# Kernel tuning notes

Hardware: AMD Instinct MI355X
Metric: run time of the kernel (lower is better)

## Reference

```python
import jax, jax.numpy as jnp
import numpy as np

B, S, H, F, E, K = 4, 2048, 1024, 3584, 8, 2
CAP_FACTOR = 1.25


def setup_inputs() -> dict:
    key = jax.random.key(0)
    k1, k2, k3, k4, k5 = jax.random.split(key, 5)
    s_h = 1.0 / np.sqrt(H)
    s_f = 1.0 / np.sqrt(F)
    return {
        "hidden_states": jax.random.normal(k1, (B, S, H), dtype=jnp.float32),
        "gate_w": jax.random.normal(k2, (E, H), dtype=jnp.float32) * s_h,
        "w1": jax.random.normal(k3, (E, H, F), dtype=jnp.float32) * s_h,
        "w2": jax.random.normal(k4, (E, F, H), dtype=jnp.float32) * s_f,
        "w3": jax.random.normal(k5, (E, H, F), dtype=jnp.float32) * s_h,
    }


def _moe_forward(hidden_states, gate_w, w1, w2, w3):
    b, s, h = hidden_states.shape
    dtype = hidden_states.dtype
    x = hidden_states.reshape(-1, h)  # [B*S, H]
    router_logits = x @ gate_w.T  # [B*S, E]
    expert_weights = jax.nn.softmax(router_logits.astype(jnp.float32), axis=1)
    _, selected_experts = jax.lax.top_k(expert_weights, K)  # [B*S, K]

    top_k_idx = selected_experts.reshape(b, s, K)
    probs = expert_weights.reshape(b, s, E)

    capacity = int(s * K / E * CAP_FACTOR)  # expert capacity per batch

    # dispatch/combine masks (Mixtral 'dropping' implementation)
    expert_mask = jax.nn.one_hot(top_k_idx, E, dtype=jnp.int32)  # [b,s,K,E]
    mask_fused = expert_mask.reshape(b, s * K, E)
    count_fused = jnp.cumsum(mask_fused, axis=1)  # running count per expert
    count = count_fused.reshape(b, s, K, E)
    trunc_mask = expert_mask * (count <= capacity).astype(jnp.int32)
    combined_mask = trunc_mask.sum(axis=2)  # [b,s,E]
    masked_probs = probs * combined_mask  # drop over-capacity tokens

    pos_fused = mask_fused * count_fused
    pos = pos_fused.reshape(b, s, K, E)
    combined_pos = pos.sum(axis=2) * combined_mask  # [b,s,E], 1-based slot
    pos_in_cap = jax.nn.one_hot(combined_pos, capacity + 1, dtype=jnp.int32)
    combine_mask = masked_probs[..., None] * pos_in_cap  # [b,s,E,cap+1]
    combine_mask = combine_mask[..., 1:].astype(dtype)  # drop slot 0 (dropped tokens)
    dispatch_mask = (combine_mask != 0).astype(dtype)  # [b,s,E,cap]

    # dispatch tokens into per-expert capacity buffers
    dispatch = jnp.einsum('bsm,bsec->ebcm', hidden_states, dispatch_mask)
    # expert FFN (SwiGLU)
    h1 = jnp.einsum('ebcm,emh->ebch', dispatch, w1)
    h3 = jnp.einsum('ebcm,emh->ebch', dispatch, w3)
    expert_out = jnp.einsum('ebch,ehm->ebcm', jax.nn.silu(h1) * h3, w2)
    # combine back to token order with routing probabilities
    final = jnp.einsum('ebcm,bsec->bsm', expert_out, combine_mask)
    return final


def reference(hidden_states, gate_w, w1, w2, w3):
    return _moe_forward(hidden_states, gate_w, w1, w2, w3)
```

## Files before the change

kernel.cpp:

```cpp
#include <hip/hip_runtime.h>
#include <hip/hip_bf16.h>
#include <math.h>

#define B_   4
#define S_   2048
#define H_   1024
#define F_   3584
#define E_   8
#define TOPK 2
#define CAP  640
#define M_   (B_*CAP)
#define NTOK (B_*S_)

typedef __attribute__((ext_vector_type(8))) short short8;
typedef __attribute__((ext_vector_type(4))) float f32x4;
typedef __attribute__((ext_vector_type(4))) unsigned short us4;

static __device__ __forceinline__ unsigned short f2bf(float f) {
  __hip_bfloat16 h = __float2bfloat16(f);
  return *reinterpret_cast<unsigned short*>(&h);
}
static __device__ __forceinline__ float bf2f(unsigned short u) {
  unsigned int x = ((unsigned int)u) << 16;
  float f;
  __builtin_memcpy(&f, &x, 4);
  return f;
}

static __device__ __forceinline__ void gload16(const void* g, void* l) {
  __builtin_amdgcn_global_load_lds((const __attribute__((address_space(1))) void*)g,
                                   (__attribute__((address_space(3))) void*)l, 16, 0, 0);
}

#define BAR() __builtin_amdgcn_s_barrier()
#define VM4() asm volatile("s_waitcnt vmcnt(4)" ::: "memory")
#define VM0() asm volatile("s_waitcnt vmcnt(0)" ::: "memory")

__global__ __launch_bounds__(64) void k_router(const float* __restrict__ hs,
                                               const float* __restrict__ gw,
                                               int* __restrict__ e01,
                                               float* __restrict__ p01,
                                               unsigned short* __restrict__ hsb) {
  int t = blockIdx.x;
  int lane = threadIdx.x;
  const float4* xv = (const float4*)(hs + (size_t)t * H_);
  float4 xr[4];
#pragma unroll
  for (int i = 0; i < 4; ++i) xr[i] = xv[lane + i * 64];
#pragma unroll
  for (int i = 0; i < 4; ++i) {
    us4 v = {f2bf(xr[i].x), f2bf(xr[i].y), f2bf(xr[i].z), f2bf(xr[i].w)};
    *(us4*)&hsb[(size_t)t * H_ + (size_t)(lane + i * 64) * 4] = v;
  }
  float logit[E_];
#pragma unroll
  for (int e = 0; e < E_; ++e) {
    const float4* gv = (const float4*)(gw + (size_t)e * H_);
    float acc = 0.f;
#pragma unroll
    for (int i = 0; i < 4; ++i) {
      float4 g = gv[lane + i * 64];
      acc += xr[i].x * g.x + xr[i].y * g.y + xr[i].z * g.z + xr[i].w * g.w;
    }
#pragma unroll
    for (int off = 32; off > 0; off >>= 1) acc += __shfl_xor(acc, off);
    logit[e] = acc;
  }
  float mx = logit[0];
#pragma unroll
  for (int e = 1; e < E_; ++e) mx = fmaxf(mx, logit[e]);
  float p[E_], s = 0.f;
#pragma unroll
  for (int e = 0; e < E_; ++e) { p[e] = expf(logit[e] - mx); s += p[e]; }
  float inv = 1.f / s;
  int e0 = 0;
#pragma unroll
  for (int e = 1; e < E_; ++e) if (p[e] > p[e0]) e0 = e;
  int e1 = (e0 == 0) ? 1 : 0;
#pragma unroll
  for (int e = 0; e < E_; ++e) if (e != e0 && p[e] > p[e1]) e1 = e;
  if (lane == 0) {
    e01[t * 2 + 0] = e0;
    e01[t * 2 + 1] = e1;
    p01[t * 2 + 0] = p[e0] * inv;
    p01[t * 2 + 1] = p[e1] * inv;
  }
}

__global__ __launch_bounds__(256) void k_positions(const int* __restrict__ e01,
                                                   int* __restrict__ pos,
                                                   int* __restrict__ disp) {
  int b = blockIdx.x, tid = threadIdx.x;
  __shared__ unsigned char eid[S_ * TOPK];
  __shared__ int part[256];
  for (int i = tid; i < E_ * CAP; i += 256)
    disp[((size_t)(i / CAP) * B_ + b) * CAP + (i % CAP)] = -1;
  for (int i = tid; i < S_ * TOPK; i += 256)
    eid[i] = (unsigned char)e01[b * S_ * TOPK + i];
  __syncthreads();
  const int per = (S_ * TOPK) / 256;
  int base = tid * per;
  for (int e = 0; e < E_; ++e) {
    int cnt = 0;
    for (int j = 0; j < per; ++j) cnt += (eid[base + j] == e) ? 1 : 0;
    part[tid] = cnt;
    __syncthreads();
    for (int off = 1; off < 256; off <<= 1) {
      int v = part[tid];
      int add = (tid >= off) ? part[tid - off] : 0;
      __syncthreads();
      part[tid] = v + add;
      __syncthreads();
    }
    int run = part[tid] - cnt;
    for (int j = 0; j < per; ++j) {
      int sl = base + j;
      if (eid[sl] == e) {
        ++run;
        int p = (run <= CAP) ? (run - 1) : -1;
        pos[b * S_ * TOPK + sl] = p;
        if (p >= 0) disp[((size_t)e * B_ + b) * CAP + p] = sl >> 1;
      }
    }
    __syncthreads();
  }
}

__global__ __launch_bounds__(256) void k_transpose(const float* __restrict__ in,
                                                   unsigned short* __restrict__ outp,
                                                   int R, int C, int ileave, int half,
                                                   size_t ostride_e) {
  __shared__ unsigned short ls[64][72];
  int e = blockIdx.z, tc = blockIdx.x, tr = blockIdx.y, tid = threadIdx.x;
  const float* src = in + (size_t)e * R * C + (size_t)tr * 64 * C + (size_t)tc * 64;
#pragma unroll
  for (int i = 0; i < 16; ++i) {
    int row = i * 4 + (tid >> 6), col = tid & 63;
    ls[row][col] = f2bf(src[(size_t)row * C + col]);
  }
  __syncthreads();
  unsigned short* dbase = outp + (size_t)e * ostride_e;
#pragma unroll
  for (int i = 0; i < 4; ++i) {
    int orow = i * 16 + (tid >> 4), oc = (tid & 15) * 4;
    int gr = tc * 64 + orow;
    int ri = ileave ? ((gr & ~15) * 2 + (gr & 15) + half * 16) : gr;
    us4 v = {ls[oc + 0][orow], ls[oc + 1][orow], ls[oc + 2][orow], ls[oc + 3][orow]};
    *(us4*)&dbase[(size_t)ri * R + tr * 64 + oc] = v;
  }
}

#define STAGE_A(d, h, t) {                                                    \
    size_t _o = (size_t)(t) * 64 + (h) * 32;                                  \
    gload16(pA0 + _o, &lds[((d) * 2 + (h)) * 8192 + tid * 8]);                \
    gload16(pA1 + _o, &lds[((d) * 2 + (h)) * 8192 + tid * 8 + 4096]);         \
  }
#define STAGE_B(d, h, t) {                                                    \
    size_t _o = (size_t)(t) * 64 + (h) * 32;                                  \
    gload16(srcB + _o, &lds[32768 + ((d) * 2 + (h)) * 8192 + tid * 8]);       \
    gload16(srcB + (size_t)128 * KTOT + _o, &lds[32768 + ((d) * 2 + (h)) * 8192 + tid * 8 + 4096]); \
  }
#define RD_A4(d, h, mh) {                                                     \
    const unsigned short* _pa = &lds[((d) * 2 + (h)) * 8192 + aoff + (mh) * 2048]; \
    _Pragma("unroll") for (int j = 0; j < 4; ++j)                             \
      a[j] = *(const short8*)&_pa[j * 512];                                   \
  }
#define RD_B4(d, h) {                                                         \
    const unsigned short* _pb = &lds[32768 + ((d) * 2 + (h)) * 8192 + boff];  \
    _Pragma("unroll") for (int n = 0; n < 4; ++n)                             \
      b[n] = *(const short8*)&_pb[n * 512];                                   \
  }
#define MFMA16(mh) {                                                          \
    __builtin_amdgcn_s_setprio(1);                                            \
    _Pragma("unroll") for (int j = 0; j < 4; ++j)                             \
      _Pragma("unroll") for (int n = 0; n < 4; ++n)                           \
        acc[(mh) * 4 + j][n] = __builtin_amdgcn_mfma_f32_16x16x32_bf16(a[j], b[n], acc[(mh) * 4 + j][n], 0, 0, 0); \
    __builtin_amdgcn_s_setprio(0);                                            \
  }
#define BODY(P, tn) {                                                         \
    RD_A4(P, 0, 0); RD_B4(P, 0); STAGE_A((P) ^ 1, 0, tn); STAGE_B((P) ^ 1, 0, tn); \
    MFMA16(0);                                                                \
    RD_A4(P, 0, 1); MFMA16(1); VM4(); BAR();                                  \
    RD_A4(P, 1, 0); RD_B4(P, 1); STAGE_A((P) ^ 1, 1, tn); STAGE_B((P) ^ 1, 1, tn); \
    MFMA16(0);                                                                \
    RD_A4(P, 1, 1); MFMA16(1); VM4(); BAR();                                  \
  }
#define PEEL(P) {                                                             \
    RD_A4(P, 0, 0); RD_B4(P, 0);                                              \
    MFMA16(0);                                                                \
    RD_A4(P, 0, 1); MFMA16(1); VM0(); BAR();                                  \
    RD_A4(P, 1, 0); RD_B4(P, 1);                                              \
    MFMA16(0);                                                                \
    RD_A4(P, 1, 1); MFMA16(1);                                                \
  }

template <int KTOT, bool SWIGLU, bool GATHER, int MT, int NTN, int NTOTB, int SPLITK>
__global__ __launch_bounds__(512, 2) void k_gemm256(const unsigned short* __restrict__ Aall,
                                                    const unsigned short* __restrict__ Ball,
                                                    unsigned short* __restrict__ Cout,
                                                    const int* __restrict__ disp) {
  constexpr int KSUB = KTOT / SPLITK;
  constexpr int NT = KSUB / 64;
  __shared__ __align__(16) unsigned short lds[65536];

  const int nwg = MT * NTN * E_ * SPLITK;
  int lid = blockIdx.x;
  int sw = (lid & 7) * (nwg >> 3) + (lid >> 3);
  constexpr int PER = MT * NTN;
  int ks = sw / (PER * E_);
  int rem2 = sw - ks * (PER * E_);
  int e = rem2 / PER;
  int rem = rem2 - e * PER;
  int tn = rem / MT, tm = rem - tn * MT;

  int tid = threadIdx.x, li = tid & 63, wid = tid >> 6;
  int wm = wid >> 2, wn = wid & 3;

  int rS = tid >> 2;
  int gS = (tid & 3) ^ ((tid >> 3) & 3);
  const unsigned short* pA0;
  const unsigned short* pA1;
  if constexpr (GATHER) {
    int r0 = tm * 256 + rS;
    int r1 = r0 + 128;
    int b0 = r0 / CAP, b1 = r1 / CAP;
    int tok0 = disp[(size_t)e * B_ * CAP + r0];
    int tok1 = disp[(size_t)e * B_ * CAP + r1];
    if (tok0 < 0) tok0 = 0;
    if (tok1 < 0) tok1 = 0;
    pA0 = Aall + ((size_t)b0 * S_ + tok0) * H_ + ks * KSUB + gS * 8;
    pA1 = Aall + ((size_t)b1 * S_ + tok1) * H_ + ks * KSUB + gS * 8;
  } else {
    const unsigned short* srcA = Aall + ((size_t)e * M_ + (size_t)tm * 256 + rS) * KTOT + ks * KSUB + gS * 8;
    pA0 = srcA;
    pA1 = srcA + (size_t)128 * KTOT;
  }
  const unsigned short* srcB = Ball + ((size_t)e * NTOTB + (size_t)tn * 256 + rS) * KTOT + ks * KSUB + gS * 8;

  int sA = (li >> 4) ^ ((li >> 1) & 3);
  int aoff = (wm * 128 + (li & 15)) * 32 + sA * 8;
  int boff = (wn * 64 + (li & 15)) * 32 + sA * 8;

  f32x4 acc[8][4] = {};
  short8 a[4], b[4];

  STAGE_A(0, 0, 0); STAGE_B(0, 0, 0);
  STAGE_A(0, 1, 0); STAGE_B(0, 1, 0);
  VM4();
  BAR();

#pragma unroll 1
  for (int t = 0; t + 1 < NT - 1; t += 2) {
    BODY(0, t + 1);
    BODY(1, t + 2);
  }
  if constexpr (((NT - 1) & 1) != 0) {
    BODY(0, NT - 1);
  }
  if constexpr (((NT - 1) & 1) != 0) {
    PEEL(1);
  } else {
    PEEL(0);
  }

  int r0o = tm * 256 + wm * 128 + ((li >> 4) << 2);
  if constexpr (SWIGLU) {
    unsigned short* out = Cout + (size_t)e * M_ * F_;
#pragma unroll
    for (int m = 0; m < 8; ++m)
#pragma unroll
      for (int u = 0; u < 2; ++u) {
        int col = (tn * 8 + wn * 2 + u) * 16 + (li & 15);
#pragma unroll
        for (int j = 0; j < 4; ++j) {
          float h1 = acc[m][2 * u][j], h3 = acc[m][2 * u + 1][j];
          float sg = 1.f / (1.f + __expf(-h1));
          out[(size_t)(r0o + m * 16 + j) * F_ + col] = f2bf(h1 * sg * h3);
        }
      }
  } else {
    unsigned short* out = Cout + ((size_t)ks * E_ + e) * M_ * NTOTB;
#pragma unroll
    for (int m = 0; m < 8; ++m)
#pragma unroll
      for (int n = 0; n < 4; ++n) {
        int col = tn * 256 + wn * 64 + n * 16 + (li & 15);
#pragma unroll
        for (int j = 0; j < 4; ++j)
          out[(size_t)(r0o + m * 16 + j) * NTOTB + col] = f2bf(acc[m][n][j]);
      }
  }
}

__global__ __launch_bounds__(256) void k_combine(const unsigned short* __restrict__ Oe0,
                                                 const unsigned short* __restrict__ Oe1,
                                                 const int* __restrict__ e01,
                                                 const float* __restrict__ p01,
                                                 const int* __restrict__ pos,
                                                 float* __restrict__ outp) {
  int t = blockIdx.x;
  int b = t / S_;
  int tid = threadIdx.x;
  float4 acc = {0.f, 0.f, 0.f, 0.f};
#pragma unroll
  for (int k = 0; k < TOPK; ++k) {
    int p = pos[t * 2 + k];
    if (p >= 0) {
      int e = e01[t * 2 + k];
      float w = p01[t * 2 + k];
      size_t row = (size_t)e * M_ + (size_t)b * CAP + p;
      us4 v0 = *(const us4*)&Oe0[row * H_ + tid * 4];
      us4 v1 = *(const us4*)&Oe1[row * H_ + tid * 4];
      acc.x += w * (bf2f(v0[0]) + bf2f(v1[0]));
      acc.y += w * (bf2f(v0[1]) + bf2f(v1[1]));
      acc.z += w * (bf2f(v0[2]) + bf2f(v1[2]));
      acc.w += w * (bf2f(v0[3]) + bf2f(v1[3]));
    }
  }
  *(float4*)&outp[(size_t)t * H_ + tid * 4] = acc;
}

extern "C" void kernel_launch(void* const* d_in, const int* in_sizes, int n_in,
                              void* d_out, int out_size, void* d_ws, size_t ws_size,
                              hipStream_t stream) {
  const float* hs = (const float*)d_in[0];
  const float* gw = (const float*)d_in[1];
  const float* w1 = (const float*)d_in[2];
  const float* w2 = (const float*)d_in[3];
  const float* w3 = (const float*)d_in[4];

  char* ws = (char*)d_ws;
  size_t off = 0;
  auto take = [&](size_t bytes) -> char* {
    char* p = ws + off;
    off += (bytes + 255) & ~(size_t)255;
    return p;
  };
  int*            e01  = (int*)take((size_t)NTOK * 2 * 4);
  float*          p01  = (float*)take((size_t)NTOK * 2 * 4);
  int*            pos  = (int*)take((size_t)NTOK * 2 * 4);
  int*            disp = (int*)take((size_t)E_ * B_ * CAP * 4);
  unsigned short* w13t = (unsigned short*)take((size_t)E_ * 2 * F_ * H_ * 2);
  unsigned short* w2t  = (unsigned short*)take((size_t)E_ * H_ * F_ * 2);
  unsigned short* hsb  = (unsigned short*)take((size_t)NTOK * H_ * 2);
  unsigned short* act  = (unsigned short*)take((size_t)E_ * M_ * F_ * 2);
  unsigned short* oe   = (unsigned short*)take((size_t)2 * E_ * M_ * H_ * 2);

  k_router<<<NTOK, 64, 0, stream>>>(hs, gw, e01, p01, hsb);
  k_positions<<<B_, 256, 0, stream>>>(e01, pos, disp);
  k_transpose<<<dim3(F_ / 64, H_ / 64, E_), 256, 0, stream>>>(w1, w13t, H_, F_, 1, 0, (size_t)2 * F_ * H_);
  k_transpose<<<dim3(F_ / 64, H_ / 64, E_), 256, 0, stream>>>(w3, w13t, H_, F_, 1, 1, (size_t)2 * F_ * H_);
  k_transpose<<<dim3(H_ / 64, F_ / 64, E_), 256, 0, stream>>>(w2, w2t, F_, H_, 0, 0, (size_t)H_ * F_);
  k_gemm256<H_, true, true, M_ / 256, (2 * F_) / 256, 2 * F_, 1>
      <<<(M_ / 256) * ((2 * F_) / 256) * E_, 512, 0, stream>>>(hsb, w13t, act, disp);
  k_gemm256<F_, false, false, M_ / 256, H_ / 256, H_, 2>
      <<<(M_ / 256) * (H_ / 256) * E_ * 2, 512, 0, stream>>>(act, w2t, oe, disp);
  k_combine<<<NTOK, 256, 0, stream>>>(oe, oe + (size_t)E_ * M_ * H_, e01, p01, pos, (float*)d_out);
}
```

Measured before the change: 583.3 us.

## Double GEMM workgroup to 1024 threads with 64x64 per-wave tiles

The expert GEMM kernel now runs 16 waves per workgroup instead of 8. Each wave owns a 64x64 output tile instead of 128x64, so the accumulator array is halved and each thread stages one A row and one B row. The inner loop is simplified to read all fragments, wait on lgkmcnt(0), then issue 16 MFMAs, dropping the old split A reads that overlapped with MFMAs. The aim is more waves per SIMD to hide memory latency. The costs are more LDS read traffic per FLOP, less overlap between LDS reads and MFMAs, and register pressure from the tighter launch bounds (1024, 4), which could cause spills.

```diff
diff --git a/kernel.cpp b/kernel.cpp
--- a/kernel.cpp
+++ b/kernel.cpp
@@ -33,7 +33,8 @@
 }
 
 #define BAR() __builtin_amdgcn_s_barrier()
-#define VM4() asm volatile("s_waitcnt vmcnt(4)" ::: "memory")
+#define WLG() asm volatile("s_waitcnt lgkmcnt(0)" ::: "memory")
+#define VM2() asm volatile("s_waitcnt vmcnt(2)" ::: "memory")
 #define VM0() asm volatile("s_waitcnt vmcnt(0)" ::: "memory")
 
 __global__ __launch_bounds__(64) void k_router(const float* __restrict__ hs,
@@ -151,54 +152,46 @@
 }
 
 #define STAGE_A(d, h, t) {                                                    \
-    size_t _o = (size_t)(t) * 64 + (h) * 32;                                  \
-    gload16(pA0 + _o, &lds[((d) * 2 + (h)) * 8192 + tid * 8]);                \
-    gload16(pA1 + _o, &lds[((d) * 2 + (h)) * 8192 + tid * 8 + 4096]);         \
+    gload16(pA0 + (size_t)(t) * 64 + (h) * 32, &lds[((d) * 2 + (h)) * 8192 + tid * 8]); \
   }
 #define STAGE_B(d, h, t) {                                                    \
-    size_t _o = (size_t)(t) * 64 + (h) * 32;                                  \
-    gload16(srcB + _o, &lds[32768 + ((d) * 2 + (h)) * 8192 + tid * 8]);       \
-    gload16(srcB + (size_t)128 * KTOT + _o, &lds[32768 + ((d) * 2 + (h)) * 8192 + tid * 8 + 4096]); \
-  }
-#define RD_A4(d, h, mh) {                                                     \
-    const unsigned short* _pa = &lds[((d) * 2 + (h)) * 8192 + aoff + (mh) * 2048]; \
-    _Pragma("unroll") for (int j = 0; j < 4; ++j)                             \
-      a[j] = *(const short8*)&_pa[j * 512];                                   \
+    gload16(srcB + (size_t)(t) * 64 + (h) * 32, &lds[32768 + ((d) * 2 + (h)) * 8192 + tid * 8]); \
+  }
+#define RD_A4(d, h) {                                                         \
+    const unsigned short* _pa = &lds[((d) * 2 + (h)) * 8192 + aoff];          \
+    _Pragma("unroll") for (int m = 0; m < 4; ++m)                             \
+      a[m] = *(const short8*)&_pa[m * 512];                                   \
   }
 #define RD_B4(d, h) {                                                         \
     const unsigned short* _pb = &lds[32768 + ((d) * 2 + (h)) * 8192 + boff];  \
     _Pragma("unroll") for (int n = 0; n < 4; ++n)                             \
       b[n] = *(const short8*)&_pb[n * 512];                                   \
   }
-#define MFMA16(mh) {                                                          \
+#define MFMA16() {                                                            \
     __builtin_amdgcn_s_setprio(1);                                            \
-    _Pragma("unroll") for (int j = 0; j < 4; ++j)                             \
+    _Pragma("unroll") for (int m = 0; m < 4; ++m)                             \
       _Pragma("unroll") for (int n = 0; n < 4; ++n)                           \
-        acc[(mh) * 4 + j][n] = __builtin_amdgcn_mfma_f32_16x16x32_bf16(a[j], b[n], acc[(mh) * 4 + j][n], 0, 0, 0); \
+        acc[m][n] = __builtin_amdgcn_mfma_f32_16x16x32_bf16(a[m], b[n], acc[m][n], 0, 0, 0); \
     __builtin_amdgcn_s_setprio(0);                                            \
   }
 #define BODY(P, tn) {                                                         \
-    RD_A4(P, 0, 0); RD_B4(P, 0); STAGE_A((P) ^ 1, 0, tn); STAGE_B((P) ^ 1, 0, tn); \
-    MFMA16(0);                                                                \
-    RD_A4(P, 0, 1); MFMA16(1); VM4(); BAR();                                  \
-    RD_A4(P, 1, 0); RD_B4(P, 1); STAGE_A((P) ^ 1, 1, tn); STAGE_B((P) ^ 1, 1, tn); \
-    MFMA16(0);                                                                \
-    RD_A4(P, 1, 1); MFMA16(1); VM4(); BAR();                                  \
+    RD_A4(P, 0); RD_B4(P, 0); STAGE_A((P) ^ 1, 0, tn); STAGE_B((P) ^ 1, 0, tn); \
+    WLG(); MFMA16(); VM2(); BAR();                                            \
+    RD_A4(P, 1); RD_B4(P, 1); STAGE_A((P) ^ 1, 1, tn); STAGE_B((P) ^ 1, 1, tn); \
+    WLG(); MFMA16(); VM2(); BAR();                                            \
   }
 #define PEEL(P) {                                                             \
-    RD_A4(P, 0, 0); RD_B4(P, 0);                                              \
-    MFMA16(0);                                                                \
-    RD_A4(P, 0, 1); MFMA16(1); VM0(); BAR();                                  \
-    RD_A4(P, 1, 0); RD_B4(P, 1);                                              \
-    MFMA16(0);                                                                \
-    RD_A4(P, 1, 1); MFMA16(1);                                                \
+    RD_A4(P, 0); RD_B4(P, 0);                                                 \
+    WLG(); MFMA16(); VM0(); BAR();                                            \
+    RD_A4(P, 1); RD_B4(P, 1);                                                 \
+    WLG(); MFMA16();                                                          \
   }
 
 template <int KTOT, bool SWIGLU, bool GATHER, int MT, int NTN, int NTOTB, int SPLITK>
-__global__ __launch_bounds__(512, 2) void k_gemm256(const unsigned short* __restrict__ Aall,
-                                                    const unsigned short* __restrict__ Ball,
-                                                    unsigned short* __restrict__ Cout,
-                                                    const int* __restrict__ disp) {
+__global__ __launch_bounds__(1024, 4) void k_gemm256(const unsigned short* __restrict__ Aall,
+                                                     const unsigned short* __restrict__ Ball,
+                                                     unsigned short* __restrict__ Cout,
+                                                     const int* __restrict__ disp) {
   constexpr int KSUB = KTOT / SPLITK;
   constexpr int NT = KSUB / 64;
   __shared__ __align__(16) unsigned short lds[65536];
@@ -219,34 +212,27 @@
   int rS = tid >> 2;
   int gS = (tid & 3) ^ ((tid >> 3) & 3);
   const unsigned short* pA0;
-  const unsigned short* pA1;
   if constexpr (GATHER) {
     int r0 = tm * 256 + rS;
-    int r1 = r0 + 128;
-    int b0 = r0 / CAP, b1 = r1 / CAP;
+    int b0 = r0 / CAP;
     int tok0 = disp[(size_t)e * B_ * CAP + r0];
-    int tok1 = disp[(size_t)e * B_ * CAP + r1];
     if (tok0 < 0) tok0 = 0;
-    if (tok1 < 0) tok1 = 0;
     pA0 = Aall + ((size_t)b0 * S_ + tok0) * H_ + ks * KSUB + gS * 8;
-    pA1 = Aall + ((size_t)b1 * S_ + tok1) * H_ + ks * KSUB + gS * 8;
   } else {
-    const unsigned short* srcA = Aall + ((size_t)e * M_ + (size_t)tm * 256 + rS) * KTOT + ks * KSUB + gS * 8;
-    pA0 = srcA;
-    pA1 = srcA + (size_t)128 * KTOT;
+    pA0 = Aall + ((size_t)e * M_ + (size_t)tm * 256 + rS) * KTOT + ks * KSUB + gS * 8;
   }
   const unsigned short* srcB = Ball + ((size_t)e * NTOTB + (size_t)tn * 256 + rS) * KTOT + ks * KSUB + gS * 8;
 
   int sA = (li >> 4) ^ ((li >> 1) & 3);
-  int aoff = (wm * 128 + (li & 15)) * 32 + sA * 8;
+  int aoff = (wm * 64 + (li & 15)) * 32 + sA * 8;
   int boff = (wn * 64 + (li & 15)) * 32 + sA * 8;
 
-  f32x4 acc[8][4] = {};
+  f32x4 acc[4][4] = {};
   short8 a[4], b[4];
 
   STAGE_A(0, 0, 0); STAGE_B(0, 0, 0);
   STAGE_A(0, 1, 0); STAGE_B(0, 1, 0);
-  VM4();
+  VM2();
   BAR();
 
 #pragma unroll 1
@@ -263,11 +249,11 @@
     PEEL(0);
   }
 
-  int r0o = tm * 256 + wm * 128 + ((li >> 4) << 2);
+  int r0o = tm * 256 + wm * 64 + ((li >> 4) << 2);
   if constexpr (SWIGLU) {
     unsigned short* out = Cout + (size_t)e * M_ * F_;
 #pragma unroll
-    for (int m = 0; m < 8; ++m)
+    for (int m = 0; m < 4; ++m)
 #pragma unroll
       for (int u = 0; u < 2; ++u) {
         int col = (tn * 8 + wn * 2 + u) * 16 + (li & 15);
@@ -281,7 +267,7 @@
   } else {
     unsigned short* out = Cout + ((size_t)ks * E_ + e) * M_ * NTOTB;
 #pragma unroll
-    for (int m = 0; m < 8; ++m)
+    for (int m = 0; m < 4; ++m)
 #pragma unroll
       for (int n = 0; n < 4; ++n) {
         int col = tn * 256 + wn * 64 + n * 16 + (li & 15);
@@ -352,8 +338,8 @@
   k_transpose<<<dim3(F_ / 64, H_ / 64, E_), 256, 0, stream>>>(w3, w13t, H_, F_, 1, 1, (size_t)2 * F_ * H_);
   k_transpose<<<dim3(H_ / 64, F_ / 64, E_), 256, 0, stream>>>(w2, w2t, F_, H_, 0, 0, (size_t)H_ * F_);
   k_gemm256<H_, true, true, M_ / 256, (2 * F_) / 256, 2 * F_, 1>
-      <<<(M_ / 256) * ((2 * F_) / 256) * E_, 512, 0, stream>>>(hsb, w13t, act, disp);
+      <<<(M_ / 256) * ((2 * F_) / 256) * E_, 1024, 0, stream>>>(hsb, w13t, act, disp);
   k_gemm256<F_, false, false, M_ / 256, H_ / 256, H_, 2>
-      <<<(M_ / 256) * (H_ / 256) * E_ * 2, 512, 0, stream>>>(act, w2t, oe, disp);
+      <<<(M_ / 256) * (H_ / 256) * E_ * 2, 1024, 0, stream>>>(act, w2t, oe, disp);
   k_combine<<<NTOK, 256, 0, stream>>>(oe, oe + (size_t)E_ * M_ * H_, e01, p01, pos, (float*)d_out);
 }
```

After: 599.2 us. 1.03x slower.
